# Kernel optimization log

Measured on AMD Instinct MI355X. Metric: run time of the kernel, lower is better.

## Reference

```python
import jax, jax.numpy as jnp
import numpy as np

S, H, NH, DS = 4096, 1024, 2, 64   # seq_len, hidden, num_heads, static_in_size
HD = H // NH                        # head_dim = 512
EPS = 1e-5                          # eqx.nn.LayerNorm default eps


def setup_inputs() -> dict:
    key = jax.random.key(0)
    ks = jax.random.split(key, 11)
    sc = lambda n: 1.0 / np.sqrt(n)
    return {
        "inputs": jax.random.normal(ks[0], (S, H), jnp.float32),
        "static_data": jax.random.normal(ks[1], (DS,), jnp.float32),
        "base_mask": jax.random.randint(ks[2], (S,), 0, 2).astype(bool),
        "Wq": jax.random.normal(ks[3], (H, H), jnp.float32) * sc(H),
        "Wk": jax.random.normal(ks[4], (H, H), jnp.float32) * sc(H),
        "Wv": jax.random.normal(ks[5], (H, H), jnp.float32) * sc(H),
        "Wo": jax.random.normal(ks[6], (H, H), jnp.float32) * sc(H),
        "Ws": jax.random.normal(ks[7], (H, DS), jnp.float32) * sc(DS),
        "bs": jax.random.normal(ks[8], (H,), jnp.float32) * 0.01,
        "ln_w": jnp.ones((H,), jnp.float32),
        "ln_b": jnp.zeros((H,), jnp.float32),
    }


def reference(inputs, static_data, base_mask, Wq, Wk, Wv, Wo, Ws, bs, ln_w, ln_b):
    # static embedding injected into keys/values
    semb = Ws @ static_data + bs                      # [H]
    kv_in = inputs + semb[None, :]                    # [S, H]

    # per-head projections (eqx Linear: y = W @ x, no bias in MHA projections)
    q = (inputs @ Wq.T).reshape(S, NH, HD)
    k = (kv_in @ Wk.T).reshape(S, NH, HD)
    v = (kv_in @ Wv.T).reshape(S, NH, HD)

    logits = jnp.einsum('qhd,khd->hqk', q, k) / np.sqrt(HD)  # [NH, S, S]

    # head 0: irregular mask (base_mask broadcast over queries); head 1: all-ones
    irregular = jnp.broadcast_to(base_mask[None, :], (S, S))
    mask = jnp.stack([irregular, jnp.ones((S, S), bool)], axis=0)  # [2, S, S]
    logits = jnp.where(mask, logits, jnp.finfo(logits.dtype).min)

    attn = jax.nn.softmax(logits, axis=-1)
    ctx = jnp.einsum('hqk,khd->qhd', attn, v).reshape(S, H)
    out = ctx @ Wo.T                                  # output projection

    # dropout_rate = 0 -> identity; residual + per-token LayerNorm
    res = out + inputs
    mu = res.mean(-1, keepdims=True)
    var = res.var(-1, keepdims=True)
    return (res - mu) / jnp.sqrt(var + EPS) * ln_w + ln_b
```

## Files before the change

### kernel.cpp

```cpp
#include <hip/hip_runtime.h>
#include <stdint.h>

#define S_LEN  4096
#define HID    1024
#define NHEAD  2
#define HDIM   512
#define NSPLIT 4
#define KS_STRIDE 520
#define LN_EPS 1e-5f

typedef __bf16 bf16x8 __attribute__((ext_vector_type(8)));
typedef float  f32x4  __attribute__((ext_vector_type(4)));

__device__ __forceinline__ float b2f(unsigned short u) {
    return __uint_as_float(((unsigned int)u) << 16);
}
__device__ __forceinline__ unsigned short f2b(float f) {
    unsigned int u = __float_as_uint(f);
    u += 0x7FFFu + ((u >> 16) & 1u);
    return (unsigned short)(u >> 16);
}

__device__ __forceinline__ void async_cp16(const void* g, void* l) {
    __builtin_amdgcn_global_load_lds(
        (const __attribute__((address_space(1))) unsigned int*)g,
        (__attribute__((address_space(3))) unsigned int*)l, 16, 0, 0);
}

__global__ void k_cvt4s(const float* __restrict__ i0, const float* __restrict__ i1,
                        const float* __restrict__ i2, const float* __restrict__ i3,
                        unsigned short* __restrict__ o0, unsigned short* __restrict__ o1,
                        unsigned short* __restrict__ o2, unsigned short* __restrict__ o3,
                        const float* __restrict__ Ws, const float* __restrict__ sd,
                        const float* __restrict__ bs, float* __restrict__ semb) {
    int z = blockIdx.y;
    if (z == 4) {
        int j = blockIdx.x * blockDim.x + threadIdx.x;
        if (j >= HID) return;
        float acc = bs[j];
        const float* row = Ws + j * 64;
        #pragma unroll
        for (int d = 0; d < 64; ++d) acc += row[d] * sd[d];
        semb[j] = acc;
        return;
    }
    const float* in = z == 0 ? i0 : z == 1 ? i1 : z == 2 ? i2 : i3;
    unsigned short* o = z == 0 ? o0 : z == 1 ? o1 : z == 2 ? o2 : o3;
    int i = (blockIdx.x * blockDim.x + threadIdx.x) * 8;
    float4 a = *(const float4*)(in + i);
    float4 b = *(const float4*)(in + i + 4);
    unsigned short r[8] = {f2b(a.x), f2b(a.y), f2b(a.z), f2b(a.w),
                           f2b(b.x), f2b(b.y), f2b(b.z), f2b(b.w)};
    *(uint4*)(o + i) = *(const uint4*)r;
}

__global__ void k_kvin(const float* __restrict__ X,
                       const float* __restrict__ semb,
                       unsigned short* __restrict__ Xb,
                       unsigned short* __restrict__ kv) {
    int idx = (blockIdx.x * blockDim.x + threadIdx.x) * 8;
    if (idx >= S_LEN * HID) return;
    int col = idx & (HID - 1);
    float4 a = *(const float4*)(X + idx);
    float4 b = *(const float4*)(X + idx + 4);
    unsigned short xo[8] = {f2b(a.x), f2b(a.y), f2b(a.z), f2b(a.w),
                            f2b(b.x), f2b(b.y), f2b(b.z), f2b(b.w)};
    *(uint4*)(Xb + idx) = *(const uint4*)xo;
    unsigned short o[8];
    o[0] = f2b(a.x + semb[col + 0]);
    o[1] = f2b(a.y + semb[col + 1]);
    o[2] = f2b(a.z + semb[col + 2]);
    o[3] = f2b(a.w + semb[col + 3]);
    o[4] = f2b(b.x + semb[col + 4]);
    o[5] = f2b(b.y + semb[col + 5]);
    o[6] = f2b(b.z + semb[col + 6]);
    o[7] = f2b(b.w + semb[col + 7]);
    *(uint4*)(kv + idx) = *(const uint4*)o;
}

__device__ __forceinline__
void gemm128(const unsigned short* __restrict__ A,
             const unsigned short* __restrict__ B,
             unsigned short* __restrict__ Cb,
             int bx, int nx, int ldc) {
    __shared__ unsigned short As[2][128 * 32];
    __shared__ unsigned short Bs[2][128 * 32];
    int tid  = threadIdx.x;
    int wave = tid >> 6, lane = tid & 63;
    int quad = lane >> 4, l16 = lane & 15;
    int wm = wave >> 1, wn = wave & 1;
    int m0 = (bx / nx) * 128, n0 = (bx % nx) * 128;

    auto stage = [&](int k0, int b) {
        #pragma unroll
        for (int i = 0; i < 2; ++i) {
            int c = tid + i * 256;
            async_cp16(A + (m0 + (c >> 2)) * HID + k0 + (c & 3) * 8, As[b] + c * 8);
            async_cp16(B + (n0 + (c >> 2)) * HID + k0 + (c & 3) * 8, Bs[b] + c * 8);
        }
    };

    f32x4 zero = {0.f, 0.f, 0.f, 0.f};
    f32x4 acc[4][4];
    #pragma unroll
    for (int i = 0; i < 4; ++i)
        #pragma unroll
        for (int j = 0; j < 4; ++j) acc[i][j] = zero;

    stage(0, 0);
    for (int it = 0; it < HID / 32; ++it) {
        int b = it & 1;
        __syncthreads();
        if (it + 1 < HID / 32) stage((it + 1) * 32, b ^ 1);

        bf16x8 af[4], bfr[4];
        #pragma unroll
        for (int i = 0; i < 4; ++i)
            af[i] = *(const bf16x8*)(As[b] + (wm * 64 + i * 16 + l16) * 32 + quad * 8);
        #pragma unroll
        for (int j = 0; j < 4; ++j)
            bfr[j] = *(const bf16x8*)(Bs[b] + (wn * 64 + j * 16 + l16) * 32 + quad * 8);
        #pragma unroll
        for (int i = 0; i < 4; ++i)
            #pragma unroll
            for (int j = 0; j < 4; ++j)
                acc[i][j] = __builtin_amdgcn_mfma_f32_16x16x32_bf16(af[i], bfr[j], acc[i][j], 0, 0, 0);
    }

    #pragma unroll
    for (int i = 0; i < 4; ++i) {
        int rbase = m0 + wm * 64 + i * 16 + quad * 4;
        #pragma unroll
        for (int j = 0; j < 4; ++j) {
            int col = n0 + wn * 64 + j * 16 + l16;
            #pragma unroll
            for (int r = 0; r < 4; ++r)
                Cb[(size_t)(rbase + r) * ldc + col] = f2b(acc[i][j][r]);
        }
    }
}

__global__ __launch_bounds__(256)
void k_gemm_qkv(const unsigned short* __restrict__ Xb,
                const unsigned short* __restrict__ kvin,
                const unsigned short* __restrict__ Wqb,
                const unsigned short* __restrict__ Wkb,
                const unsigned short* __restrict__ Wvb,
                unsigned short* __restrict__ Qb,
                unsigned short* __restrict__ Kb,
                unsigned short* __restrict__ Vt) {
    int bx = (blockIdx.x & 7) * 32 + (blockIdx.x >> 3);
    int z = blockIdx.z;
    if (z == 0)      gemm128(Xb,   Wqb,  Qb,  bx,  8, HID);
    else if (z == 1) gemm128(kvin, Wkb,  Kb,  bx,  8, HID);
    else             gemm128(Wvb,  kvin, Vt,  bx, 32, S_LEN);
}

__global__ __launch_bounds__(256)
void k_gemm_o(const unsigned short* __restrict__ Opart,
              const float* __restrict__ Lbuf,
              const unsigned short* __restrict__ B,
              float* __restrict__ Cf,
              const float* __restrict__ Xres) {
    __shared__ unsigned short As[2][64 * 32];
    __shared__ unsigned short Bs[2][128 * 32];
    const size_t SH = (size_t)S_LEN * HID;
    int tid  = threadIdx.x;
    int wave = tid >> 6, lane = tid & 63;
    int quad = lane >> 4, l16 = lane & 15;
    int bx = (blockIdx.x & 7) * 64 + (blockIdx.x >> 3);
    int m0 = (bx >> 3) * 64, n0 = (bx & 7) * 128;

    int arow  = m0 + (tid >> 2);
    int acol8 = (tid & 3) * 8;
    float rinv[NHEAD];
    #pragma unroll
    for (int h = 0; h < NHEAD; ++h) {
        float l = 0.f;
        #pragma unroll
        for (int z = 0; z < NSPLIT; ++z)
            l += Lbuf[(z * NHEAD + h) * S_LEN + arow];
        rinv[h] = 1.f / l;
    }

    auto stageB = [&](int k0, int b) {
        #pragma unroll
        for (int i = 0; i < 2; ++i) {
            int c = tid + i * 256;
            async_cp16(B + (n0 + (c >> 2)) * HID + k0 + (c & 3) * 8, Bs[b] + c * 8);
        }
    };
    auto stageA = [&](int k0, int b) {
        float rv = rinv[k0 >> 9];
        const unsigned short* ap = Opart + (size_t)arow * HID + k0 + acol8;
        float s[8] = {0.f, 0.f, 0.f, 0.f, 0.f, 0.f, 0.f, 0.f};
        #pragma unroll
        for (int z = 0; z < NSPLIT; ++z) {
            uint4 v = *(const uint4*)(ap + z * SH);
            unsigned short us[8];
            *(uint4*)us = v;
            #pragma unroll
            for (int e = 0; e < 8; ++e) s[e] += b2f(us[e]);
        }
        unsigned short o8[8];
        #pragma unroll
        for (int e = 0; e < 8; ++e) o8[e] = f2b(s[e] * rv);
        *(uint4*)(As[b] + tid * 8) = *(const uint4*)o8;
    };

    f32x4 zero = {0.f, 0.f, 0.f, 0.f};
    f32x4 acc[4][2];
    #pragma unroll
    for (int i = 0; i < 4; ++i)
        #pragma unroll
        for (int j = 0; j < 2; ++j) acc[i][j] = zero;

    stageB(0, 0);
    stageA(0, 0);
    for (int it = 0; it < HID / 32; ++it) {
        int b = it & 1;
        __syncthreads();
        if (it + 1 < HID / 32) {
            stageB((it + 1) * 32, b ^ 1);
            stageA((it + 1) * 32, b ^ 1);
        }
        bf16x8 af[4], bfr[2];
        #pragma unroll
        for (int i = 0; i < 4; ++i)
            af[i] = *(const bf16x8*)(As[b] + (i * 16 + l16) * 32 + quad * 8);
        #pragma unroll
        for (int j = 0; j < 2; ++j)
            bfr[j] = *(const bf16x8*)(Bs[b] + (wave * 32 + j * 16 + l16) * 32 + quad * 8);
        #pragma unroll
        for (int i = 0; i < 4; ++i)
            #pragma unroll
            for (int j = 0; j < 2; ++j)
                acc[i][j] = __builtin_amdgcn_mfma_f32_16x16x32_bf16(af[i], bfr[j], acc[i][j], 0, 0, 0);
    }

    #pragma unroll
    for (int i = 0; i < 4; ++i) {
        int rbase = m0 + i * 16 + quad * 4;
        #pragma unroll
        for (int j = 0; j < 2; ++j) {
            int col = n0 + wave * 32 + j * 16 + l16;
            #pragma unroll
            for (int r = 0; r < 4; ++r) {
                size_t o = (size_t)(rbase + r) * HID + col;
                Cf[o] = acc[i][j][r] + Xres[o];
            }
        }
    }
}

__global__ __launch_bounds__(512, 2)
void k_flash(const unsigned short* __restrict__ Q,
             const unsigned short* __restrict__ K,
             const unsigned short* __restrict__ Vt,
             const int* __restrict__ mask,
             unsigned short* __restrict__ Opart,
             float* __restrict__ Lbuf) {
    __shared__ unsigned short Ks[2][32 * KS_STRIDE];
    __shared__ __bf16 Ps[2][128][40];
    int tid  = threadIdx.x;
    int wave = tid >> 6, lane = tid & 63;
    int quad = lane >> 4, l16 = lane & 15;
    int head = blockIdx.x / NSPLIT, split = blockIdx.x % NSPLIT, qtile = blockIdx.y;

    int qrow = qtile * 128 + wave * 16 + l16;
    const unsigned short* qp = Q + qrow * HID + head * HDIM;
    bf16x8 qf[16];
    #pragma unroll
    for (int t = 0; t < 16; ++t) qf[t] = *(const bf16x8*)(qp + t * 32 + quad * 8);

    float lsum[4];
    #pragma unroll
    for (int r = 0; r < 4; ++r) lsum[r] = 0.f;
    f32x4 zero = {0.f, 0.f, 0.f, 0.f};
    f32x4 oacc[8][4];
    #pragma unroll
    for (int mt = 0; mt < 8; ++mt)
        #pragma unroll
        for (int nt = 0; nt < 4; ++nt) oacc[mt][nt] = zero;

    const float scale = 0.044194173824159216f;
    const unsigned short* Kbase = K + head * HDIM;
    const unsigned short* vptr = Vt + (size_t)(head * HDIM + wave * 64 + l16) * S_LEN
                                    + split * 1024 + quad * 8;

    auto stageK = [&](int kt, int buf) {
        int kb = split * 1024 + kt * 32;
        #pragma unroll
        for (int i = 0; i < 4; ++i) {
            int c = tid + i * 512;
            int row = c >> 6, col = (c & 63) * 8;
            async_cp16(Kbase + (kb + row) * HID + col, &Ks[buf][row * KS_STRIDE + col]);
        }
    };

    stageK(0, 0);
    int mk0 = 1, mk1 = 1;
    if (head == 0) {
        mk0 = mask[split * 1024 + l16];
        mk1 = mask[split * 1024 + 16 + l16];
    }

    bf16x8 vf[4];
    for (int it = 0; it < 32; ++it) {
        int cur = it & 1;
        __syncthreads();

        if (it < 31) stageK(it + 1, cur ^ 1);

        __builtin_amdgcn_s_setprio(1);
        if (it > 0) {
            #pragma unroll
            for (int mt = 0; mt < 8; ++mt) {
                bf16x8 pf = *(const bf16x8*)&Ps[cur ^ 1][mt * 16 + l16][quad * 8];
                #pragma unroll
                for (int nt = 0; nt < 4; ++nt)
                    oacc[mt][nt] = __builtin_amdgcn_mfma_f32_16x16x32_bf16(pf, vf[nt], oacc[mt][nt], 0, 0, 0);
            }
        }

        #pragma unroll
        for (int nt = 0; nt < 4; ++nt)
            vf[nt] = *(const bf16x8*)(vptr + (size_t)nt * 16 * S_LEN + it * 32);

        f32x4 sacc[2];
        sacc[0] = zero; sacc[1] = zero;
        #pragma unroll
        for (int nt = 0; nt < 2; ++nt)
            #pragma unroll
            for (int t = 0; t < 16; ++t) {
                bf16x8 kf = *(const bf16x8*)&Ks[cur][(nt * 16 + l16) * KS_STRIDE + t * 32 + quad * 8];
                sacc[nt] = __builtin_amdgcn_mfma_f32_16x16x32_bf16(qf[t], kf, sacc[nt], 0, 0, 0);
            }
        __builtin_amdgcn_s_setprio(0);

        bool keep0 = mk0 != 0;
        bool keep1 = mk1 != 0;
        #pragma unroll
        for (int r = 0; r < 4; ++r) {
            float p0 = keep0 ? __expf(fminf(sacc[0][r] * scale, 30.f)) : 0.f;
            float p1 = keep1 ? __expf(fminf(sacc[1][r] * scale, 30.f)) : 0.f;
            lsum[r] += p0 + p1;
            Ps[cur][wave * 16 + quad * 4 + r][l16]      = (__bf16)p0;
            Ps[cur][wave * 16 + quad * 4 + r][16 + l16] = (__bf16)p1;
        }

        if (head == 0 && it < 31) {
            int kn = split * 1024 + (it + 1) * 32;
            mk0 = mask[kn + l16];
            mk1 = mask[kn + 16 + l16];
        }
    }

    __syncthreads();
    #pragma unroll
    for (int mt = 0; mt < 8; ++mt) {
        bf16x8 pf = *(const bf16x8*)&Ps[1][mt * 16 + l16][quad * 8];
        #pragma unroll
        for (int nt = 0; nt < 4; ++nt)
            oacc[mt][nt] = __builtin_amdgcn_mfma_f32_16x16x32_bf16(pf, vf[nt], oacc[mt][nt], 0, 0, 0);
    }

    #pragma unroll
    for (int r = 0; r < 4; ++r) {
        float s = lsum[r];
        #pragma unroll
        for (int off = 1; off < 16; off <<= 1)
            s += __shfl_xor(s, off, 64);
        lsum[r] = s;
    }
    int lrow = qtile * 128 + wave * 16 + quad * 4;
    if (l16 == 0) {
        #pragma unroll
        for (int r = 0; r < 4; ++r)
            Lbuf[(split * NHEAD + head) * S_LEN + lrow + r] = lsum[r];
    }
    unsigned short* op = Opart + (size_t)split * S_LEN * HID;
    #pragma unroll
    for (int mt = 0; mt < 8; ++mt)
        #pragma unroll
        for (int nt = 0; nt < 4; ++nt)
            #pragma unroll
            for (int r = 0; r < 4; ++r)
                op[(qtile * 128 + mt * 16 + quad * 4 + r) * HID +
                   head * HDIM + wave * 64 + nt * 16 + l16] = f2b(oacc[mt][nt][r]);
}

__global__ __launch_bounds__(256)
void k_ln(const float* __restrict__ res,
          const float* __restrict__ w,
          const float* __restrict__ b,
          float* __restrict__ out) {
    __shared__ float red[8];
    int s = blockIdx.x, tid = threadIdx.x;
    const float* row = res + s * HID;
    float x[4], s1 = 0.f, s2 = 0.f;
    #pragma unroll
    for (int i = 0; i < 4; ++i) {
        x[i] = row[tid + i * 256];
        s1 += x[i]; s2 += x[i] * x[i];
    }
    #pragma unroll
    for (int off = 1; off < 64; off <<= 1) {
        s1 += __shfl_xor(s1, off, 64);
        s2 += __shfl_xor(s2, off, 64);
    }
    int wave = tid >> 6;
    if ((tid & 63) == 0) { red[wave] = s1; red[4 + wave] = s2; }
    __syncthreads();
    s1 = red[0] + red[1] + red[2] + red[3];
    s2 = red[4] + red[5] + red[6] + red[7];
    float mu   = s1 * (1.f / HID);
    float var  = s2 * (1.f / HID) - mu * mu;
    float rstd = rsqrtf(var + LN_EPS);
    #pragma unroll
    for (int i = 0; i < 4; ++i) {
        int col = tid + i * 256;
        out[s * HID + col] = (x[i] - mu) * rstd * w[col] + b[col];
    }
}

extern "C" void kernel_launch(void* const* d_in, const int* in_sizes, int n_in,
                              void* d_out, int out_size, void* d_ws, size_t ws_size,
                              hipStream_t stream) {
    const float* X   = (const float*)d_in[0];
    const float* sd  = (const float*)d_in[1];
    const int*   msk = (const int*)d_in[2];
    const float* Wq  = (const float*)d_in[3];
    const float* Wk  = (const float*)d_in[4];
    const float* Wv  = (const float*)d_in[5];
    const float* Wo  = (const float*)d_in[6];
    const float* Wsp = (const float*)d_in[7];
    const float* bsp = (const float*)d_in[8];
    const float* lw  = (const float*)d_in[9];
    const float* lb  = (const float*)d_in[10];
    float* out = (float*)d_out;

    char* ws = (char*)d_ws;
    const size_t MB = 1ull << 20;
    float*          semb  = (float*)(ws);
    float*          Lbuf  = (float*)(ws + (1ull << 16));
    unsigned short* Xb    = (unsigned short*)(ws + 1 * MB);
    unsigned short* kvin  = (unsigned short*)(ws + 9 * MB);
    unsigned short* Qb    = (unsigned short*)(ws + 17 * MB);
    unsigned short* Kb    = (unsigned short*)(ws + 25 * MB);
    unsigned short* Vt    = (unsigned short*)(ws + 33 * MB);
    unsigned short* Wqb   = (unsigned short*)(ws + 49 * MB);
    unsigned short* Wkb   = (unsigned short*)(ws + 51 * MB);
    unsigned short* Wvb   = (unsigned short*)(ws + 53 * MB);
    unsigned short* Wob   = (unsigned short*)(ws + 55 * MB);
    float*          resf  = (float*)(ws + 17 * MB);
    unsigned short* Opart = (unsigned short*)(ws + 57 * MB);

    const int SH = S_LEN * HID;
    const int WW = HID * HID;

    k_cvt4s<<<dim3(WW / 8 / 256, 5), dim3(256), 0, stream>>>(
        Wq, Wk, Wv, Wo, Wqb, Wkb, Wvb, Wob, Wsp, sd, bsp, semb);

    k_kvin<<<dim3(SH / 8 / 256), dim3(256), 0, stream>>>(X, semb, Xb, kvin);

    k_gemm_qkv<<<dim3(256, 1, 3), dim3(256), 0, stream>>>(Xb, kvin, Wqb, Wkb, Wvb, Qb, Kb, Vt);

    k_flash<<<dim3(NHEAD * NSPLIT, S_LEN / 128), dim3(512), 0, stream>>>(
        Qb, Kb, Vt, msk, Opart, Lbuf);

    k_gemm_o<<<dim3(512), dim3(256), 0, stream>>>(Opart, Lbuf, Wob, resf, X);
    k_ln<<<dim3(S_LEN), dim3(256), 0, stream>>>(resf, lw, lb, out);
}
```

Before: 270.4 us.

## Compact unmasked keys for head 0 and rebalance split-K across heads

Builds a compacted index list of unmasked key positions. It gathers K and transposed V for head 0 into dense padded buffers so flash attention only iterates over active keys. The split work is rebalanced to 3 splits for head 0 and 5 splits for head 1, and the partial-output layout is made per-head. This removes the roughly half of head-0 attention work spent on masked keys. It costs an extra gather kernel, a single-block serial prefix scan, and dependence on the mask density for load balance.

```diff
diff --git a/kernel.cpp b/kernel.cpp
--- a/kernel.cpp
+++ b/kernel.cpp
@@ -5,9 +5,10 @@
 #define HID    1024
 #define NHEAD  2
 #define HDIM   512
-#define NSPLIT 4
 #define KS_STRIDE 520
 #define LN_EPS 1e-5f
+#define PADK   4224
+#define CH1    832
 
 typedef __bf16 bf16x8 __attribute__((ext_vector_type(8)));
 typedef float  f32x4  __attribute__((ext_vector_type(4)));
@@ -32,7 +33,9 @@
                         unsigned short* __restrict__ o0, unsigned short* __restrict__ o1,
                         unsigned short* __restrict__ o2, unsigned short* __restrict__ o3,
                         const float* __restrict__ Ws, const float* __restrict__ sd,
-                        const float* __restrict__ bs, float* __restrict__ semb) {
+                        const float* __restrict__ bs, float* __restrict__ semb,
+                        const int* __restrict__ msk, int* __restrict__ cidx,
+                        int* __restrict__ nactp) {
     int z = blockIdx.y;
     if (z == 4) {
         int j = blockIdx.x * blockDim.x + threadIdx.x;
@@ -42,6 +45,28 @@
         #pragma unroll
         for (int d = 0; d < 64; ++d) acc += row[d] * sd[d];
         semb[j] = acc;
+        return;
+    }
+    if (z == 5) {
+        if (blockIdx.x != 0) return;
+        __shared__ int cnts[256];
+        __shared__ int bases[256];
+        int t = threadIdx.x;
+        int c = 0;
+        #pragma unroll
+        for (int i = 0; i < 16; ++i) c += (msk[t * 16 + i] != 0);
+        cnts[t] = c;
+        __syncthreads();
+        if (t == 0) {
+            int b = 0;
+            for (int k = 0; k < 256; ++k) { bases[k] = b; b += cnts[k]; }
+            nactp[0] = b;
+        }
+        __syncthreads();
+        int b = bases[t];
+        #pragma unroll
+        for (int i = 0; i < 16; ++i)
+            if (msk[t * 16 + i] != 0) cidx[b++] = t * 16 + i;
         return;
     }
     const float* in = z == 0 ? i0 : z == 1 ? i1 : z == 2 ? i2 : i3;
@@ -157,6 +182,33 @@
 }
 
 __global__ __launch_bounds__(256)
+void k_gather(const unsigned short* __restrict__ Kb,
+              const unsigned short* __restrict__ Vt,
+              const int* __restrict__ cidx,
+              const int* __restrict__ nactp,
+              unsigned short* __restrict__ Kc,
+              unsigned short* __restrict__ Vtc) {
+    int nact = nactp[0];
+    int gid = blockIdx.x * 256 + threadIdx.x;
+    int idx = gid * 8;
+    if (blockIdx.y == 0) {
+        int j = idx >> 9, d = idx & 511;
+        uint4 v = {0u, 0u, 0u, 0u};
+        if (j < nact) v = *(const uint4*)(Kb + (size_t)cidx[j] * HID + d);
+        *(uint4*)(Kc + (size_t)j * 512 + d) = v;
+    } else {
+        int d = idx / PADK, j0 = idx % PADK;
+        unsigned short o[8];
+        #pragma unroll
+        for (int i = 0; i < 8; ++i) {
+            int j = j0 + i;
+            o[i] = (j < nact) ? Vt[(size_t)d * S_LEN + cidx[j]] : (unsigned short)0;
+        }
+        *(uint4*)(Vtc + (size_t)d * PADK + j0) = *(const uint4*)o;
+    }
+}
+
+__global__ __launch_bounds__(256)
 void k_gemm_o(const unsigned short* __restrict__ Opart,
               const float* __restrict__ Lbuf,
               const unsigned short* __restrict__ B,
@@ -164,7 +216,7 @@
               const float* __restrict__ Xres) {
     __shared__ unsigned short As[2][64 * 32];
     __shared__ unsigned short Bs[2][128 * 32];
-    const size_t SH = (size_t)S_LEN * HID;
+    const size_t SH2 = (size_t)S_LEN * 512;
     int tid  = threadIdx.x;
     int wave = tid >> 6, lane = tid & 63;
     int quad = lane >> 4, l16 = lane & 15;
@@ -174,13 +226,13 @@
     int arow  = m0 + (tid >> 2);
     int acol8 = (tid & 3) * 8;
     float rinv[NHEAD];
-    #pragma unroll
-    for (int h = 0; h < NHEAD; ++h) {
-        float l = 0.f;
-        #pragma unroll
-        for (int z = 0; z < NSPLIT; ++z)
-            l += Lbuf[(z * NHEAD + h) * S_LEN + arow];
-        rinv[h] = 1.f / l;
+    {
+        float l0 = Lbuf[arow] + Lbuf[S_LEN + arow] + Lbuf[2 * S_LEN + arow];
+        float l1 = 0.f;
+        #pragma unroll
+        for (int z = 3; z < 8; ++z) l1 += Lbuf[z * S_LEN + arow];
+        rinv[0] = 1.f / l0;
+        rinv[1] = 1.f / l1;
     }
 
     auto stageB = [&](int k0, int b) {
@@ -191,12 +243,14 @@
         }
     };
     auto stageA = [&](int k0, int b) {
-        float rv = rinv[k0 >> 9];
-        const unsigned short* ap = Opart + (size_t)arow * HID + k0 + acol8;
+        int h = k0 >> 9;
+        float rv = rinv[h];
+        int lk = (k0 & 511) + acol8;
+        const unsigned short* ap = Opart + (h ? 3 * SH2 : 0) + (size_t)arow * 512 + lk;
         float s[8] = {0.f, 0.f, 0.f, 0.f, 0.f, 0.f, 0.f, 0.f};
-        #pragma unroll
-        for (int z = 0; z < NSPLIT; ++z) {
-            uint4 v = *(const uint4*)(ap + z * SH);
+        int nz = h ? 5 : 3;
+        for (int z = 0; z < nz; ++z) {
+            uint4 v = *(const uint4*)(ap + (size_t)z * SH2);
             unsigned short us[8];
             *(uint4*)us = v;
             #pragma unroll
@@ -255,9 +309,11 @@
 
 __global__ __launch_bounds__(512, 2)
 void k_flash(const unsigned short* __restrict__ Q,
-             const unsigned short* __restrict__ K,
+             const unsigned short* __restrict__ Kb,
              const unsigned short* __restrict__ Vt,
-             const int* __restrict__ mask,
+             const unsigned short* __restrict__ Kc,
+             const unsigned short* __restrict__ Vtc,
+             const int* __restrict__ nactp,
              unsigned short* __restrict__ Opart,
              float* __restrict__ Lbuf) {
     __shared__ unsigned short Ks[2][32 * KS_STRIDE];
@@ -265,7 +321,25 @@
     int tid  = threadIdx.x;
     int wave = tid >> 6, lane = tid & 63;
     int quad = lane >> 4, l16 = lane & 15;
-    int head = blockIdx.x / NSPLIT, split = blockIdx.x % NSPLIT, qtile = blockIdx.y;
+    int x = blockIdx.x, qtile = blockIdx.y;
+    int head  = (x >= 3) ? 1 : 0;
+    int split = head ? x - 3 : x;
+    int nact  = nactp[0];
+
+    int nit, base, krs, vrs;
+    const unsigned short *Ksrc, *Vsrc;
+    if (head == 0) {
+        nit  = (nact + 95) / 96;
+        base = split * nit * 32;
+        Ksrc = Kc;  krs = 512;
+        Vsrc = Vtc; vrs = PADK;
+    } else {
+        base = split * CH1;
+        nit  = min(CH1 >> 5, (S_LEN - base) >> 5);
+        Ksrc = Kb + HDIM;  krs = HID;
+        Vsrc = Vt + (size_t)HDIM * S_LEN;
+        vrs  = S_LEN;
+    }
 
     int qrow = qtile * 128 + wave * 16 + l16;
     const unsigned short* qp = Q + qrow * HID + head * HDIM;
@@ -284,33 +358,26 @@
         for (int nt = 0; nt < 4; ++nt) oacc[mt][nt] = zero;
 
     const float scale = 0.044194173824159216f;
-    const unsigned short* Kbase = K + head * HDIM;
-    const unsigned short* vptr = Vt + (size_t)(head * HDIM + wave * 64 + l16) * S_LEN
-                                    + split * 1024 + quad * 8;
+    const unsigned short* vptr = Vsrc + (size_t)(wave * 64 + l16) * vrs + base + quad * 8;
 
     auto stageK = [&](int kt, int buf) {
-        int kb = split * 1024 + kt * 32;
+        int kb = base + kt * 32;
         #pragma unroll
         for (int i = 0; i < 4; ++i) {
             int c = tid + i * 512;
             int row = c >> 6, col = (c & 63) * 8;
-            async_cp16(Kbase + (kb + row) * HID + col, &Ks[buf][row * KS_STRIDE + col]);
+            async_cp16(Ksrc + (size_t)(kb + row) * krs + col, &Ks[buf][row * KS_STRIDE + col]);
         }
     };
 
-    stageK(0, 0);
-    int mk0 = 1, mk1 = 1;
-    if (head == 0) {
-        mk0 = mask[split * 1024 + l16];
-        mk1 = mask[split * 1024 + 16 + l16];
-    }
+    if (nit > 0) stageK(0, 0);
 
     bf16x8 vf[4];
-    for (int it = 0; it < 32; ++it) {
+    for (int it = 0; it < nit; ++it) {
         int cur = it & 1;
         __syncthreads();
 
-        if (it < 31) stageK(it + 1, cur ^ 1);
+        if (it + 1 < nit) stageK(it + 1, cur ^ 1);
 
         __builtin_amdgcn_s_setprio(1);
         if (it > 0) {
@@ -325,7 +392,7 @@
 
         #pragma unroll
         for (int nt = 0; nt < 4; ++nt)
-            vf[nt] = *(const bf16x8*)(vptr + (size_t)nt * 16 * S_LEN + it * 32);
+            vf[nt] = *(const bf16x8*)(vptr + (size_t)nt * 16 * vrs + it * 32);
 
         f32x4 sacc[2];
         sacc[0] = zero; sacc[1] = zero;
@@ -338,8 +405,12 @@
             }
         __builtin_amdgcn_s_setprio(0);
 
-        bool keep0 = mk0 != 0;
-        bool keep1 = mk1 != 0;
+        bool keep0 = true, keep1 = true;
+        if (head == 0) {
+            int kb = base + it * 32;
+            keep0 = kb + l16 < nact;
+            keep1 = kb + 16 + l16 < nact;
+        }
         #pragma unroll
         for (int r = 0; r < 4; ++r) {
             float p0 = keep0 ? __expf(fminf(sacc[0][r] * scale, 30.f)) : 0.f;
@@ -348,21 +419,18 @@
             Ps[cur][wave * 16 + quad * 4 + r][l16]      = (__bf16)p0;
             Ps[cur][wave * 16 + quad * 4 + r][16 + l16] = (__bf16)p1;
         }
-
-        if (head == 0 && it < 31) {
-            int kn = split * 1024 + (it + 1) * 32;
-            mk0 = mask[kn + l16];
-            mk1 = mask[kn + 16 + l16];
-        }
-    }
-
-    __syncthreads();
-    #pragma unroll
-    for (int mt = 0; mt < 8; ++mt) {
-        bf16x8 pf = *(const bf16x8*)&Ps[1][mt * 16 + l16][quad * 8];
-        #pragma unroll
-        for (int nt = 0; nt < 4; ++nt)
-            oacc[mt][nt] = __builtin_amdgcn_mfma_f32_16x16x32_bf16(pf, vf[nt], oacc[mt][nt], 0, 0, 0);
+    }
+
+    if (nit > 0) {
+        int lastb = (nit - 1) & 1;
+        __syncthreads();
+        #pragma unroll
+        for (int mt = 0; mt < 8; ++mt) {
+            bf16x8 pf = *(const bf16x8*)&Ps[lastb][mt * 16 + l16][quad * 8];
+            #pragma unroll
+            for (int nt = 0; nt < 4; ++nt)
+                oacc[mt][nt] = __builtin_amdgcn_mfma_f32_16x16x32_bf16(pf, vf[nt], oacc[mt][nt], 0, 0, 0);
+        }
     }
 
     #pragma unroll
@@ -373,21 +441,22 @@
             s += __shfl_xor(s, off, 64);
         lsum[r] = s;
     }
+    int slot = head ? 3 + split : split;
     int lrow = qtile * 128 + wave * 16 + quad * 4;
     if (l16 == 0) {
         #pragma unroll
         for (int r = 0; r < 4; ++r)
-            Lbuf[(split * NHEAD + head) * S_LEN + lrow + r] = lsum[r];
-    }
-    unsigned short* op = Opart + (size_t)split * S_LEN * HID;
+            Lbuf[slot * S_LEN + lrow + r] = lsum[r];
+    }
+    unsigned short* op = Opart + (size_t)slot * S_LEN * 512;
     #pragma unroll
     for (int mt = 0; mt < 8; ++mt)
         #pragma unroll
         for (int nt = 0; nt < 4; ++nt)
             #pragma unroll
             for (int r = 0; r < 4; ++r)
-                op[(qtile * 128 + mt * 16 + quad * 4 + r) * HID +
-                   head * HDIM + wave * 64 + nt * 16 + l16] = f2b(oacc[mt][nt][r]);
+                op[(qtile * 128 + mt * 16 + quad * 4 + r) * 512 +
+                   wave * 64 + nt * 16 + l16] = f2b(oacc[mt][nt][r]);
 }
 
 __global__ __launch_bounds__(256)
@@ -443,9 +512,13 @@
     char* ws = (char*)d_ws;
     const size_t MB = 1ull << 20;
     float*          semb  = (float*)(ws);
+    int*            cidx  = (int*)(ws + (16 << 10));
+    int*            nactp = (int*)(ws + (48 << 10));
     float*          Lbuf  = (float*)(ws + (1ull << 16));
     unsigned short* Xb    = (unsigned short*)(ws + 1 * MB);
     unsigned short* kvin  = (unsigned short*)(ws + 9 * MB);
+    unsigned short* Kc    = (unsigned short*)(ws + 1 * MB);
+    unsigned short* Vtc   = (unsigned short*)(ws + 5 * MB + (256 << 10));
     unsigned short* Qb    = (unsigned short*)(ws + 17 * MB);
     unsigned short* Kb    = (unsigned short*)(ws + 25 * MB);
     unsigned short* Vt    = (unsigned short*)(ws + 33 * MB);
@@ -459,15 +532,18 @@
     const int SH = S_LEN * HID;
     const int WW = HID * HID;
 
-    k_cvt4s<<<dim3(WW / 8 / 256, 5), dim3(256), 0, stream>>>(
-        Wq, Wk, Wv, Wo, Wqb, Wkb, Wvb, Wob, Wsp, sd, bsp, semb);
+    k_cvt4s<<<dim3(WW / 8 / 256, 6), dim3(256), 0, stream>>>(
+        Wq, Wk, Wv, Wo, Wqb, Wkb, Wvb, Wob, Wsp, sd, bsp, semb, msk, cidx, nactp);
 
     k_kvin<<<dim3(SH / 8 / 256), dim3(256), 0, stream>>>(X, semb, Xb, kvin);
 
     k_gemm_qkv<<<dim3(256, 1, 3), dim3(256), 0, stream>>>(Xb, kvin, Wqb, Wkb, Wvb, Qb, Kb, Vt);
 
-    k_flash<<<dim3(NHEAD * NSPLIT, S_LEN / 128), dim3(512), 0, stream>>>(
-        Qb, Kb, Vt, msk, Opart, Lbuf);
+    k_gather<<<dim3(PADK * 512 / 8 / 256, 2), dim3(256), 0, stream>>>(
+        Kb, Vt, cidx, nactp, Kc, Vtc);
+
+    k_flash<<<dim3(8, S_LEN / 128), dim3(512), 0, stream>>>(
+        Qb, Kb, Vt, Kc, Vtc, nactp, Opart, Lbuf);
 
     k_gemm_o<<<dim3(512), dim3(256), 0, stream>>>(Opart, Lbuf, Wob, resf, X);
     k_ln<<<dim3(S_LEN), dim3(256), 0, stream>>>(resf, lw, lb, out);
```

Result: no change. 270.3 us (-0.1%).
